# Optimization experiments

Hardware: AMD Instinct MI355X
Metric: run time of the kernel (lower is better)

Reference implementation:

```python
import jax, jax.numpy as jnp
import numpy as np

N_NODES = 50000
N_EDGES = 640000
N_REL = 200
D_IN = 128
D_OUT = 128


def setup_inputs() -> dict:
    key = jax.random.key(0)
    k1, k2, k3, k4, k5, k6 = jax.random.split(key, 6)
    x = jax.random.normal(k1, (N_NODES, D_IN), dtype=jnp.float32)
    edge_index = jax.random.randint(k2, (2, N_EDGES), 0, N_NODES, dtype=jnp.int64)
    edge_type = jax.random.randint(k3, (N_EDGES,), 0, N_REL, dtype=jnp.int64)
    rel_emb = jax.random.normal(k4, (N_REL, D_IN), dtype=jnp.float32)
    # nn.Linear weights stored as [out_features, in_features]
    W_lin = jax.random.normal(k5, (D_OUT, D_IN), dtype=jnp.float32) * (1.0 / np.sqrt(D_IN))
    # xavier_uniform for attn kernel [1, D_IN]
    limit = np.sqrt(6.0 / (1 + D_IN))
    W_attn = jax.random.uniform(k6, (1, D_IN), dtype=jnp.float32, minval=-limit, maxval=limit)
    return {"x": x, "edge_index": edge_index, "edge_type": edge_type,
            "rel_emb": rel_emb, "W_lin": W_lin, "W_attn": W_attn}


def reference(x, edge_index, edge_type, rel_emb, W_lin, W_attn):
    # x: [N, D_in]; edge_index: [2, E]; edge_type: [E]; rel_emb: [R, D_in]
    x_trans = x @ W_lin.T                       # [N, D_out]
    src_idx, tgt_idx = edge_index[0], edge_index[1]
    h_src = x[src_idx]                          # [E, D_in] gather
    h_rel = rel_emb[edge_type]                  # [E, D_in] gather
    sum_feat = h_src + h_rel                    # [E, D_in]
    attn = jax.nn.sigmoid(sum_feat @ W_attn.T)  # [E, 1]
    msg = x_trans[src_idx] * attn               # [E, D_out]
    out = jax.ops.segment_sum(msg, tgt_idx, num_segments=x.shape[0])  # [N, D_out]
    return jax.nn.relu(out)
```

## Files before the change

### kernel.cpp

```cpp
#include <hip/hip_runtime.h>
#include <hip/hip_bf16.h>

#define N_NODES 50000
#define N_EDGES 640000
#define N_REL   200
#define D       128
#define CAP     64

typedef __attribute__((ext_vector_type(8))) short short8;
typedef __attribute__((ext_vector_type(4))) float floatx4;

__device__ __forceinline__ unsigned short f2bf(float f) {
    unsigned u = __float_as_uint(f);
    u += 0x7FFF + ((u >> 16) & 1);
    return (unsigned short)(u >> 16);
}

__device__ __forceinline__ float sigmoidf(float x) {
    return 1.f / (1.f + __expf(-x));
}

__global__ void setup_kernel(const float* __restrict__ W,
                             const float* __restrict__ x,
                             const float* __restrict__ rel,
                             const float* __restrict__ Wattn,
                             unsigned short* __restrict__ Wbf,
                             float* __restrict__ s_rel,
                             float* __restrict__ s_node,
                             int* __restrict__ count) {
    const int b = blockIdx.x;
    if (b < 64) {
        const int i = b * 256 + threadIdx.x;
        Wbf[i] = f2bf(W[i]);
    } else if (b < 114) {
        const int wave = (b - 64) * 4 + (threadIdx.x >> 6);
        const int lane = threadIdx.x & 63;
        if (wave < N_REL) {
            const float* __restrict__ row = rel + (size_t)wave * D;
            float a = fmaf(row[lane], Wattn[lane],
                           row[lane + 64] * Wattn[lane + 64]);
#pragma unroll
            for (int off = 32; off; off >>= 1)
                a += __shfl_down(a, off);
            if (lane == 0) s_rel[wave] = a;
        }
    } else if (b < 310) {
        const int i = (b - 114) * 256 + threadIdx.x;
        if (i < N_NODES) count[i] = 0;
    } else {
        const int node = (b - 310) * 8 + (threadIdx.x >> 5);
        const int sub  = threadIdx.x & 31;
        if (node < N_NODES) {
            const float4 xv = ((const float4*)(x + (size_t)node * D))[sub];
            const float4 wv = ((const float4*)Wattn)[sub];
            float a = xv.x * wv.x + xv.y * wv.y + xv.z * wv.z + xv.w * wv.w;
#pragma unroll
            for (int off = 16; off; off >>= 1)
                a += __shfl_xor(a, off);
            if (sub == 0) s_node[node] = a;
        }
    }
}

__global__ void fused_kernel(const float* __restrict__ x,
                             const unsigned short* __restrict__ Wbf,
                             unsigned short* __restrict__ xt,
                             const int* __restrict__ src_idx,
                             const int* __restrict__ tgt_idx,
                             const int* __restrict__ etype,
                             const float* __restrict__ s_node,
                             const float* __restrict__ s_rel,
                             int* __restrict__ count,
                             unsigned* __restrict__ sorted) {
    const int b = blockIdx.x;
    if ((b & 3) == 3) {
        const int wid = (b >> 2) * 4 + (threadIdx.x >> 6);
        if (wid >= N_NODES / 16) return;
        const int lane = threadIdx.x & 63;
        const int r16  = lane & 15;
        const int quad = lane >> 4;
        const int m0   = wid * 16;

        short8 af[4];
#pragma unroll
        for (int s = 0; s < 4; ++s) {
            const int k0 = s * 32 + quad * 8;
            const float* __restrict__ xr = x + (size_t)(m0 + r16) * D + k0;
            const float4 lo = *(const float4*)(xr);
            const float4 hi = *(const float4*)(xr + 4);
            short8 a;
            a[0] = (short)f2bf(lo.x); a[1] = (short)f2bf(lo.y);
            a[2] = (short)f2bf(lo.z); a[3] = (short)f2bf(lo.w);
            a[4] = (short)f2bf(hi.x); a[5] = (short)f2bf(hi.y);
            a[6] = (short)f2bf(hi.z); a[7] = (short)f2bf(hi.w);
            af[s] = a;
        }

#pragma unroll
        for (int t = 0; t < 8; ++t) {
            floatx4 acc = {0.f, 0.f, 0.f, 0.f};
#pragma unroll
            for (int s = 0; s < 4; ++s) {
                const int k0 = s * 32 + quad * 8;
                const short8 bb = *(const short8*)(Wbf + (size_t)(t * 16 + r16) * D + k0);
                acc = __builtin_amdgcn_mfma_f32_16x16x32_bf16(af[s], bb, acc, 0, 0, 0);
            }
#pragma unroll
            for (int r = 0; r < 4; ++r) {
                const int orow = m0 + quad * 4 + r;
                xt[(size_t)orow * D + t * 16 + r16] = f2bf(acc[r]);
            }
        }
    } else {
        const int sb = b - (b >> 2);
        const int e = sb * 256 + threadIdx.x;
        if (e >= N_EDGES) return;
        const int s = src_idx[e];
        const int t = tgt_idx[e];
        const int r = etype[e];

        const float logit = s_node[s] + s_rel[r];
        const unsigned rec = ((unsigned)f2bf(sigmoidf(logit)) << 16) | (unsigned)s;

        const int k = atomicAdd(&count[t], 1);
        sorted[t * CAP + k] = rec;
    }
}

__device__ __forceinline__ void gproc(unsigned r, const unsigned short* __restrict__ xt,
                                      int sub, float4& acc) {
    const unsigned src = r & 0xFFFFu;
    const float a = __uint_as_float(r & 0xFFFF0000u);
    const uint2 p = *(const uint2*)(xt + (size_t)src * D + sub * 4);
    acc.x = fmaf(a, __uint_as_float(p.x << 16),        acc.x);
    acc.y = fmaf(a, __uint_as_float(p.x & 0xFFFF0000u), acc.y);
    acc.z = fmaf(a, __uint_as_float(p.y << 16),        acc.z);
    acc.w = fmaf(a, __uint_as_float(p.y & 0xFFFF0000u), acc.w);
}

__global__ void gather_kernel(const int* __restrict__ count,
                              const unsigned* __restrict__ sorted,
                              const unsigned short* __restrict__ xt,
                              float* __restrict__ out) {
    const int wid  = (blockIdx.x * blockDim.x + threadIdx.x) >> 6;
    const int lane = threadIdx.x & 63;
    const int half = lane >> 5;
    const int sub  = lane & 31;
    const int t    = wid * 2 + half;
    if (t >= N_NODES) return;

    const int cnt = count[t];
    const unsigned* __restrict__ rec = sorted + (size_t)t * CAP;

    float4 acc = {0.f, 0.f, 0.f, 0.f};
    int i = 0;
    for (; i + 4 <= cnt; i += 4) {
        const uint4 r4 = *(const uint4*)(rec + i);
        gproc(r4.x, xt, sub, acc);
        gproc(r4.y, xt, sub, acc);
        gproc(r4.z, xt, sub, acc);
        gproc(r4.w, xt, sub, acc);
    }
    for (; i < cnt; ++i)
        gproc(rec[i], xt, sub, acc);

    float4 o;
    o.x = fmaxf(acc.x, 0.f);
    o.y = fmaxf(acc.y, 0.f);
    o.z = fmaxf(acc.z, 0.f);
    o.w = fmaxf(acc.w, 0.f);
    ((float4*)(out + (size_t)t * D))[sub] = o;
}

extern "C" void kernel_launch(void* const* d_in, const int* in_sizes, int n_in,
                              void* d_out, int out_size, void* d_ws, size_t ws_size,
                              hipStream_t stream) {
    const float* x        = (const float*)d_in[0];
    const int*   edge_idx = (const int*)d_in[1];
    const int*   etype    = (const int*)d_in[2];
    const float* rel_emb  = (const float*)d_in[3];
    const float* W_lin    = (const float*)d_in[4];
    const float* W_attn   = (const float*)d_in[5];
    float* out = (float*)d_out;

    const int* src_idx = edge_idx;
    const int* tgt_idx = edge_idx + N_EDGES;

    unsigned short* xt   = (unsigned short*)d_ws;
    float* s_node        = (float*)(xt + (size_t)N_NODES * D);
    float* s_rel         = s_node + N_NODES;
    unsigned short* Wbf  = (unsigned short*)(s_rel + N_REL);
    int*   count         = (int*)(Wbf + D * D);
    unsigned* sorted     = (unsigned*)(count + N_NODES);

    setup_kernel<<<dim3(310 + (N_NODES + 7) / 8), dim3(256), 0, stream>>>(
        W_lin, x, rel_emb, W_attn, Wbf, s_rel, s_node, count);

    fused_kernel<<<dim3(3333), dim3(256), 0, stream>>>(
        x, Wbf, xt, src_idx, tgt_idx, etype, s_node, s_rel, count, sorted);

    gather_kernel<<<dim3(N_NODES / 8), dim3(256), 0, stream>>>(
        count, sorted, xt, out);
}
```

Baseline: 176.0 us.

## Split fused kernel; partition edge scatter by target-node range for locality

The combined GEMM/edge-scatter kernel is split into a separate MFMA transform kernel and a scatter kernel. In the new scatter kernel, each block reads a chunk of edges and only handles those whose target falls in one of eight node ranges. Atomics and record writes from one block therefore land in a narrower address window, which should improve cache locality. The cost is that every edge's target index is read eight times, plus an extra launch and the loss of overlap between the GEMM and the scatter.

```diff
diff --git a/kernel.cpp b/kernel.cpp
--- a/kernel.cpp
+++ b/kernel.cpp
@@ -6,6 +6,10 @@
 #define N_REL   200
 #define D       128
 #define CAP     64
+#define RANGES  8
+#define NODES_PER_RANGE (N_NODES / RANGES)
+#define CHUNK_EDGES 2560
+#define N_CHUNKS (N_EDGES / CHUNK_EDGES)
 
 typedef __attribute__((ext_vector_type(8))) short short8;
 typedef __attribute__((ext_vector_type(4))) float floatx4;
@@ -62,68 +66,73 @@
     }
 }
 
-__global__ void fused_kernel(const float* __restrict__ x,
-                             const unsigned short* __restrict__ Wbf,
-                             unsigned short* __restrict__ xt,
-                             const int* __restrict__ src_idx,
-                             const int* __restrict__ tgt_idx,
-                             const int* __restrict__ etype,
-                             const float* __restrict__ s_node,
-                             const float* __restrict__ s_rel,
-                             int* __restrict__ count,
-                             unsigned* __restrict__ sorted) {
-    const int b = blockIdx.x;
-    if ((b & 3) == 3) {
-        const int wid = (b >> 2) * 4 + (threadIdx.x >> 6);
-        if (wid >= N_NODES / 16) return;
-        const int lane = threadIdx.x & 63;
-        const int r16  = lane & 15;
-        const int quad = lane >> 4;
-        const int m0   = wid * 16;
-
-        short8 af[4];
+__global__ void xtrans_mfma_kernel(const float* __restrict__ x,
+                                   const unsigned short* __restrict__ Wbf,
+                                   unsigned short* __restrict__ xt) {
+    const int wid = (blockIdx.x * blockDim.x + threadIdx.x) >> 6;
+    if (wid >= N_NODES / 16) return;
+    const int lane = threadIdx.x & 63;
+    const int r16  = lane & 15;
+    const int quad = lane >> 4;
+    const int m0   = wid * 16;
+
+    short8 af[4];
+#pragma unroll
+    for (int s = 0; s < 4; ++s) {
+        const int k0 = s * 32 + quad * 8;
+        const float* __restrict__ xr = x + (size_t)(m0 + r16) * D + k0;
+        const float4 lo = *(const float4*)(xr);
+        const float4 hi = *(const float4*)(xr + 4);
+        short8 a;
+        a[0] = (short)f2bf(lo.x); a[1] = (short)f2bf(lo.y);
+        a[2] = (short)f2bf(lo.z); a[3] = (short)f2bf(lo.w);
+        a[4] = (short)f2bf(hi.x); a[5] = (short)f2bf(hi.y);
+        a[6] = (short)f2bf(hi.z); a[7] = (short)f2bf(hi.w);
+        af[s] = a;
+    }
+
+#pragma unroll
+    for (int t = 0; t < 8; ++t) {
+        floatx4 acc = {0.f, 0.f, 0.f, 0.f};
 #pragma unroll
         for (int s = 0; s < 4; ++s) {
             const int k0 = s * 32 + quad * 8;
-            const float* __restrict__ xr = x + (size_t)(m0 + r16) * D + k0;
-            const float4 lo = *(const float4*)(xr);
-            const float4 hi = *(const float4*)(xr + 4);
-            short8 a;
-            a[0] = (short)f2bf(lo.x); a[1] = (short)f2bf(lo.y);
-            a[2] = (short)f2bf(lo.z); a[3] = (short)f2bf(lo.w);
-            a[4] = (short)f2bf(hi.x); a[5] = (short)f2bf(hi.y);
-            a[6] = (short)f2bf(hi.z); a[7] = (short)f2bf(hi.w);
-            af[s] = a;
-        }
-
-#pragma unroll
-        for (int t = 0; t < 8; ++t) {
-            floatx4 acc = {0.f, 0.f, 0.f, 0.f};
-#pragma unroll
-            for (int s = 0; s < 4; ++s) {
-                const int k0 = s * 32 + quad * 8;
-                const short8 bb = *(const short8*)(Wbf + (size_t)(t * 16 + r16) * D + k0);
-                acc = __builtin_amdgcn_mfma_f32_16x16x32_bf16(af[s], bb, acc, 0, 0, 0);
-            }
-#pragma unroll
-            for (int r = 0; r < 4; ++r) {
-                const int orow = m0 + quad * 4 + r;
-                xt[(size_t)orow * D + t * 16 + r16] = f2bf(acc[r]);
-            }
-        }
-    } else {
-        const int sb = b - (b >> 2);
-        const int e = sb * 256 + threadIdx.x;
-        if (e >= N_EDGES) return;
-        const int s = src_idx[e];
+            const short8 b = *(const short8*)(Wbf + (size_t)(t * 16 + r16) * D + k0);
+            acc = __builtin_amdgcn_mfma_f32_16x16x32_bf16(af[s], b, acc, 0, 0, 0);
+        }
+#pragma unroll
+        for (int r = 0; r < 4; ++r) {
+            const int orow = m0 + quad * 4 + r;
+            xt[(size_t)orow * D + t * 16 + r16] = f2bf(acc[r]);
+        }
+    }
+}
+
+__global__ void scatter_kernel(const int* __restrict__ src_idx,
+                               const int* __restrict__ tgt_idx,
+                               const int* __restrict__ etype,
+                               const float* __restrict__ s_node,
+                               const float* __restrict__ s_rel,
+                               int* __restrict__ count,
+                               unsigned* __restrict__ sorted) {
+    const int b     = blockIdx.x;
+    const int lo    = (b & 7) * NODES_PER_RANGE;
+    const int hi    = lo + NODES_PER_RANGE;
+    const int base  = (b >> 3) * CHUNK_EDGES + threadIdx.x;
+
+#pragma unroll
+    for (int it = 0; it < CHUNK_EDGES / 256; ++it) {
+        const int e = base + it * 256;
         const int t = tgt_idx[e];
-        const int r = etype[e];
-
-        const float logit = s_node[s] + s_rel[r];
-        const unsigned rec = ((unsigned)f2bf(sigmoidf(logit)) << 16) | (unsigned)s;
-
-        const int k = atomicAdd(&count[t], 1);
-        sorted[t * CAP + k] = rec;
+        if (t >= lo && t < hi) {
+            const int s = src_idx[e];
+            const int r = etype[e];
+            const float logit = s_node[s] + s_rel[r];
+            const unsigned rec =
+                ((unsigned)f2bf(sigmoidf(logit)) << 16) | (unsigned)s;
+            const int k = atomicAdd(&count[t], 1);
+            sorted[t * CAP + k] = rec;
+        }
     }
 }
 
@@ -196,8 +205,11 @@
     setup_kernel<<<dim3(310 + (N_NODES + 7) / 8), dim3(256), 0, stream>>>(
         W_lin, x, rel_emb, W_attn, Wbf, s_rel, s_node, count);
 
-    fused_kernel<<<dim3(3333), dim3(256), 0, stream>>>(
-        x, Wbf, xt, src_idx, tgt_idx, etype, s_node, s_rel, count, sorted);
+    xtrans_mfma_kernel<<<dim3((N_NODES / 16 * 64 + 255) / 256), dim3(256), 0, stream>>>(
+        x, Wbf, xt);
+
+    scatter_kernel<<<dim3(N_CHUNKS * RANGES), dim3(256), 0, stream>>>(
+        src_idx, tgt_idx, etype, s_node, s_rel, count, sorted);
 
     gather_kernel<<<dim3(N_NODES / 8), dim3(256), 0, stream>>>(
         count, sorted, xt, out);
```

After: 169.2 us. 1.04x faster.
